# Optimization experiments

Hardware: AMD Instinct MI355X
Metric: run time of the kernel (lower is better)

## Reference

```python
import jax, jax.numpy as jnp
import numpy as np

H = 16            # num heads (sharded)
NOPE = 128        # qk_nope_head_dim
ROPE = 64         # qk_rope_head_dim
VD = 128          # v_head_dim
KV_RANK = 512
HEAD = NOPE + ROPE  # 192
SCALE = HEAD ** (-0.5)  # mscale == 1 (no yarn scaling)
EPS = 1e-6


def rmsnorm(x, w):
    var = jnp.mean(x * x, axis=-1, keepdims=True)
    return x * jax.lax.rsqrt(var + EPS) * w


def apply_rope(pe, cos, sin):
    # pe: [T, h, ROPE]; torch code de-interleaves pairs then applies
    # non-interleaved (rotate-half) rope: out = [e*cos - o*sin, o*cos + e*sin]
    e = pe[..., 0::2]
    o = pe[..., 1::2]
    c = cos[:, None, :]
    s = sin[:, None, :]
    return jnp.concatenate([e * c - o * s, o * c + e * s], axis=-1)


def setup_inputs() -> dict:
    key = jax.random.key(0)
    ks = jax.random.split(key, 10)
    T, D = 4096, 2048
    w = 0.02
    return {
        "hidden_states": jax.random.normal(ks[0], (T, D), jnp.float32),
        "cos": jax.random.uniform(ks[1], (T, ROPE // 2), jnp.float32),
        "sin": jax.random.uniform(ks[2], (T, ROPE // 2), jnp.float32),
        "w_q_a": jax.random.normal(ks[3], (D, 1536), jnp.float32) * w,
        "q_a_ln_w": jnp.ones((1536,), jnp.float32),
        "w_q_b": jax.random.normal(ks[4], (1536, H * HEAD), jnp.float32) * w,
        "w_kv_a": jax.random.normal(ks[5], (D, KV_RANK + ROPE), jnp.float32) * w,
        "kv_a_ln_w": jnp.ones((KV_RANK,), jnp.float32),
        "w_kv_b": jax.random.normal(ks[6], (KV_RANK, H * (NOPE + VD)), jnp.float32) * w,
        "w_o": jax.random.normal(ks[7], (H * VD, D), jnp.float32) * w,
        "batch_size": 2,
    }


def reference(hidden_states, cos, sin, w_q_a, q_a_ln_w, w_q_b, w_kv_a,
              kv_a_ln_w, w_kv_b, w_o, batch_size):
    T, D = hidden_states.shape
    B = int(batch_size)
    S = T // B

    # Q: low-rank down proj -> RMSNorm -> up proj
    q = rmsnorm(hidden_states @ w_q_a, q_a_ln_w) @ w_q_b
    q = q.reshape(T, H, HEAD)
    q_nope = q[..., :NOPE]
    q_pe = apply_rope(q[..., NOPE:], cos, sin)

    # KV: joint down proj with shared rope part (MQA-style)
    ckv = hidden_states @ w_kv_a                        # [T, 512+64]
    compressed_kv = ckv[:, :KV_RANK]
    k_pe = apply_rope(ckv[:, KV_RANK:][:, None, :], cos, sin)  # [T, 1, 64]
    kv = (rmsnorm(compressed_kv, kv_a_ln_w) @ w_kv_b).reshape(T, H, NOPE + VD)
    k_nope = kv[..., :NOPE]
    v = kv[..., NOPE:]                                   # [T, H, 128]

    # Assemble full query/key heads (value pad to 192 + final slice is a no-op
    # mathematically since padded dims are zero; we keep value dim = 128).
    query = jnp.concatenate([q_nope, q_pe], axis=-1)     # [T, H, 192]
    key = jnp.concatenate([k_nope, jnp.broadcast_to(k_pe, (T, H, ROPE))], axis=-1)

    # Causal (prefill) attention per sequence
    qb = query.reshape(B, S, H, HEAD)
    kb = key.reshape(B, S, H, HEAD)
    vb = v.reshape(B, S, H, VD)
    scores = jnp.einsum("bqhd,bkhd->bhqk", qb, kb) * SCALE
    causal = jnp.tril(jnp.ones((S, S), bool))
    scores = jnp.where(causal, scores, jnp.finfo(scores.dtype).min)
    probs = jax.nn.softmax(scores, axis=-1)
    attn = jnp.einsum("bhqk,bkhd->bqhd", probs, vb)      # [B, S, H, 128]

    return attn.reshape(T, H * VD) @ w_o
```

## Files before the change

kernel.cpp:

```cpp
#include <hip/hip_runtime.h>
#include <cstdint>
#include <cstddef>

#define TT 4096
#define DD 2048
#define NH 16
#define HEADD 192
#define NOPE 128
#define VDIM 128
#define SEQ 2048

typedef __bf16 bf16x8 __attribute__((ext_vector_type(8)));
typedef float f32x4 __attribute__((ext_vector_type(4)));
typedef unsigned int u32;

__device__ __forceinline__ float bf2f(unsigned short u) {
    union { unsigned int i; float f; } v; v.i = ((unsigned int)u) << 16; return v.f;
}
__device__ __forceinline__ unsigned short f2bf(float f) {
    union { float f; unsigned int i; } v; v.f = f;
    unsigned int r = v.i + 0x7FFFu + ((v.i >> 16) & 1u);
    return (unsigned short)(r >> 16);
}
__device__ __forceinline__ u32 pack2bf(float a, float b) {
    return (u32)f2bf(a) | ((u32)f2bf(b) << 16);
}
__device__ __forceinline__ void gload16(const unsigned short* g, unsigned short* l) {
    __builtin_amdgcn_global_load_lds((const __attribute__((address_space(1))) u32*)g,
                                     (__attribute__((address_space(3))) u32*)l, 16, 0, 0);
}

__global__ __launch_bounds__(256) void cvt_bf16_k(const float* __restrict__ x,
                                                  unsigned short* __restrict__ y, int n) {
    int i = (blockIdx.x * 256 + threadIdx.x) * 4;
    if (i < n) {
        float4 v = *(const float4*)(x + i);
        uint2 o;
        o.x = pack2bf(v.x, v.y);
        o.y = pack2bf(v.z, v.w);
        *(uint2*)(y + i) = o;
    }
}

__global__ __launch_bounds__(256) void transpose_cvt_k(const float* __restrict__ W,
                                                       unsigned short* __restrict__ Wt,
                                                       int K, int N) {
    __shared__ float tile[32][33];
    int n0 = blockIdx.x * 32, k0 = blockIdx.y * 32;
    int t = threadIdx.x, lr = t >> 5, lc = t & 31;
#pragma unroll
    for (int p = 0; p < 4; p++) {
        int k = k0 + lr + p * 8, n = n0 + lc;
        tile[lr + p * 8][lc] = (k < K && n < N) ? W[(size_t)k * N + n] : 0.f;
    }
    __syncthreads();
#pragma unroll
    for (int p = 0; p < 4; p++) {
        int n = n0 + lr + p * 8, k = k0 + lc;
        if (n < N && k < K) Wt[(size_t)n * K + k] = f2bf(tile[lc][lr + p * 8]);
    }
}

__global__ __launch_bounds__(256) void gemm_bf16_k(const unsigned short* __restrict__ A,
                                                   const unsigned short* __restrict__ Bt,
                                                   float* __restrict__ C,
                                                   int M, int N, int K) {
    __shared__ __align__(16) unsigned short As[128 * 32];
    __shared__ __align__(16) unsigned short Bs[128 * 32];
    int bm = blockIdx.y * 128, bn = blockIdx.x * 128;
    int t = threadIdx.x;
    int wave = t >> 6, lane = t & 63;
    int wr = (wave >> 1) * 64, wc = (wave & 1) * 64;
    int l15 = lane & 15, quad = lane >> 4;
    f32x4 acc[4][4];
    f32x4 zero = {0.f, 0.f, 0.f, 0.f};
#pragma unroll
    for (int i = 0; i < 4; i++)
#pragma unroll
        for (int j = 0; j < 4; j++) acc[i][j] = zero;
    int r0 = 16 * (2 * wave) + (lane >> 2);
    int cOff = (lane & 3) * 8;
    const unsigned short* gA0 = A + (size_t)(bm + r0) * K + cOff;
    const unsigned short* gA1 = A + (size_t)(bm + r0 + 16) * K + cOff;
    const unsigned short* gB0 = Bt + (size_t)(bn + r0) * K + cOff;
    const unsigned short* gB1 = Bt + (size_t)(bn + r0 + 16) * K + cOff;
    unsigned short* lA0 = &As[(2 * wave) * 512];
    unsigned short* lA1 = &As[(2 * wave + 1) * 512];
    unsigned short* lB0 = &Bs[(2 * wave) * 512];
    unsigned short* lB1 = &Bs[(2 * wave + 1) * 512];
    for (int k0 = 0; k0 < K; k0 += 32) {
        gload16(gA0 + k0, lA0);
        gload16(gA1 + k0, lA1);
        gload16(gB0 + k0, lB0);
        gload16(gB1 + k0, lB1);
        __syncthreads();
        bf16x8 af[4], bfr[4];
#pragma unroll
        for (int i = 0; i < 4; i++)
            af[i] = *(const bf16x8*)&As[(wr + i * 16 + l15) * 32 + quad * 8];
#pragma unroll
        for (int j = 0; j < 4; j++)
            bfr[j] = *(const bf16x8*)&Bs[(wc + j * 16 + l15) * 32 + quad * 8];
#pragma unroll
        for (int i = 0; i < 4; i++)
#pragma unroll
            for (int j = 0; j < 4; j++)
                acc[i][j] = __builtin_amdgcn_mfma_f32_16x16x32_bf16(af[i], bfr[j], acc[i][j], 0, 0, 0);
        __syncthreads();
    }
#pragma unroll
    for (int i = 0; i < 4; i++) {
        int row = bm + wr + i * 16 + quad * 4;
#pragma unroll
        for (int j = 0; j < 4; j++) {
            int col = bn + wc + j * 16 + l15;
            if (col < N) {
                float* cp = C + (size_t)row * N + col;
#pragma unroll
                for (int r = 0; r < 4; r++) cp[(size_t)r * N] = acc[i][j][r];
            }
        }
    }
}

__global__ __launch_bounds__(256) void gemm_bf16o_k(const unsigned short* __restrict__ A,
                                                    const unsigned short* __restrict__ Bt,
                                                    unsigned short* __restrict__ C,
                                                    int M, int N, int K) {
    __shared__ __align__(16) unsigned short As[128 * 32];
    __shared__ __align__(16) unsigned short Bs[128 * 32];
    int bm = blockIdx.y * 128, bn = blockIdx.x * 128;
    int t = threadIdx.x;
    int wave = t >> 6, lane = t & 63;
    int wr = (wave >> 1) * 64, wc = (wave & 1) * 64;
    int l15 = lane & 15, quad = lane >> 4;
    f32x4 acc[4][4];
    f32x4 zero = {0.f, 0.f, 0.f, 0.f};
#pragma unroll
    for (int i = 0; i < 4; i++)
#pragma unroll
        for (int j = 0; j < 4; j++) acc[i][j] = zero;
    int r0 = 16 * (2 * wave) + (lane >> 2);
    int cOff = (lane & 3) * 8;
    const unsigned short* gA0 = A + (size_t)(bm + r0) * K + cOff;
    const unsigned short* gA1 = A + (size_t)(bm + r0 + 16) * K + cOff;
    const unsigned short* gB0 = Bt + (size_t)(bn + r0) * K + cOff;
    const unsigned short* gB1 = Bt + (size_t)(bn + r0 + 16) * K + cOff;
    unsigned short* lA0 = &As[(2 * wave) * 512];
    unsigned short* lA1 = &As[(2 * wave + 1) * 512];
    unsigned short* lB0 = &Bs[(2 * wave) * 512];
    unsigned short* lB1 = &Bs[(2 * wave + 1) * 512];
    for (int k0 = 0; k0 < K; k0 += 32) {
        gload16(gA0 + k0, lA0);
        gload16(gA1 + k0, lA1);
        gload16(gB0 + k0, lB0);
        gload16(gB1 + k0, lB1);
        __syncthreads();
        bf16x8 af[4], bfr[4];
#pragma unroll
        for (int i = 0; i < 4; i++)
            af[i] = *(const bf16x8*)&As[(wr + i * 16 + l15) * 32 + quad * 8];
#pragma unroll
        for (int j = 0; j < 4; j++)
            bfr[j] = *(const bf16x8*)&Bs[(wc + j * 16 + l15) * 32 + quad * 8];
#pragma unroll
        for (int i = 0; i < 4; i++)
#pragma unroll
            for (int j = 0; j < 4; j++)
                acc[i][j] = __builtin_amdgcn_mfma_f32_16x16x32_bf16(af[i], bfr[j], acc[i][j], 0, 0, 0);
        __syncthreads();
    }
#pragma unroll
    for (int i = 0; i < 4; i++) {
        int row = bm + wr + i * 16 + quad * 4;
#pragma unroll
        for (int j = 0; j < 4; j++) {
            int col = bn + wc + j * 16 + l15;
            if (col < N) {
                unsigned short* cp = C + (size_t)row * N + col;
#pragma unroll
                for (int r = 0; r < 4; r++) cp[(size_t)r * N] = f2bf(acc[i][j][r]);
            }
        }
    }
}

#define KS_STRIDE 200
#define VT_STRIDE 72

__global__ __launch_bounds__(256) void gemm_kv_k(const unsigned short* __restrict__ A,
                                                 const unsigned short* __restrict__ Bt,
                                                 unsigned short* __restrict__ Kb2,
                                                 unsigned short* __restrict__ Vt2) {
    const int K = 512;
    __shared__ __align__(16) unsigned short As[128 * 32];
    __shared__ __align__(16) unsigned short Bs[128 * 32];
    int bm = blockIdx.y * 128, bn = blockIdx.x * 128;
    int t = threadIdx.x;
    int wave = t >> 6, lane = t & 63;
    int wr = (wave >> 1) * 64, wc = (wave & 1) * 64;
    int l15 = lane & 15, quad = lane >> 4;
    f32x4 acc[4][4];
    f32x4 zero = {0.f, 0.f, 0.f, 0.f};
#pragma unroll
    for (int i = 0; i < 4; i++)
#pragma unroll
        for (int j = 0; j < 4; j++) acc[i][j] = zero;
    int r0 = 16 * (2 * wave) + (lane >> 2);
    int cOff = (lane & 3) * 8;
    const unsigned short* gA0 = A + (size_t)(bm + r0) * K + cOff;
    const unsigned short* gA1 = A + (size_t)(bm + r0 + 16) * K + cOff;
    const unsigned short* gB0 = Bt + (size_t)(bn + r0) * K + cOff;
    const unsigned short* gB1 = Bt + (size_t)(bn + r0 + 16) * K + cOff;
    unsigned short* lA0 = &As[(2 * wave) * 512];
    unsigned short* lA1 = &As[(2 * wave + 1) * 512];
    unsigned short* lB0 = &Bs[(2 * wave) * 512];
    unsigned short* lB1 = &Bs[(2 * wave + 1) * 512];
    for (int k0 = 0; k0 < K; k0 += 32) {
        gload16(gA0 + k0, lA0);
        gload16(gA1 + k0, lA1);
        gload16(gB0 + k0, lB0);
        gload16(gB1 + k0, lB1);
        __syncthreads();
        bf16x8 af[4], bfr[4];
#pragma unroll
        for (int i = 0; i < 4; i++)
            af[i] = *(const bf16x8*)&As[(wr + i * 16 + l15) * 32 + quad * 8];
#pragma unroll
        for (int j = 0; j < 4; j++)
            bfr[j] = *(const bf16x8*)&Bs[(wc + j * 16 + l15) * 32 + quad * 8];
#pragma unroll
        for (int i = 0; i < 4; i++)
#pragma unroll
            for (int j = 0; j < 4; j++)
                acc[i][j] = __builtin_amdgcn_mfma_f32_16x16x32_bf16(af[i], bfr[j], acc[i][j], 0, 0, 0);
        __syncthreads();
    }
#pragma unroll
    for (int j = 0; j < 4; j++) {
        int col = bn + wc + j * 16 + l15;
        int h = col >> 8, dd = col & 255;
#pragma unroll
        for (int i = 0; i < 4; i++) {
            int row0 = bm + wr + i * 16 + quad * 4;
#pragma unroll
            for (int r = 0; r < 4; r++) {
                int row = row0 + r;
                int b = row >> 11, s = row & 2047;
                int kt = s >> 6, sr = s & 63;
                size_t bh = (size_t)(b * NH + h);
                unsigned short v = f2bf(acc[i][j][r]);
                if (dd < 128)
                    Kb2[((bh * 32 + kt) * 64 + sr) * KS_STRIDE + dd] = v;
                else
                    Vt2[((bh * 32 + kt) * 128 + (dd - 128)) * VT_STRIDE + sr] = v;
            }
        }
    }
}

__global__ __launch_bounds__(256) void kpe_fill_k(const unsigned short* __restrict__ kpe,
                                                  unsigned short* __restrict__ Kb2) {
    int trow = blockIdx.x, t = threadIdx.x;
    int b = trow >> 11, s = trow & 2047;
    int kt = s >> 6, sr = s & 63;
    const unsigned short* src = kpe + trow * 64;
#pragma unroll
    for (int i = t; i < NH * 64; i += 256) {
        int h = i >> 6, d = i & 63;
        Kb2[(((size_t)(b * NH + h) * 32 + kt) * 64 + sr) * KS_STRIDE + 128 + d] = src[d];
    }
}

__global__ __launch_bounds__(256) void rmsnorm_bf_k(const unsigned short* __restrict__ x,
                                                    const float* __restrict__ w,
                                                    unsigned short* __restrict__ y) {
    int row = blockIdx.x, t = threadIdx.x;
    const unsigned short* xr = x + (size_t)row * 2112;
    float s = 0.f;
    for (int i = t; i < 1536; i += 256) { float v = bf2f(xr[i]); s += v * v; }
    __shared__ float red[256];
    red[t] = s; __syncthreads();
    for (int o = 128; o > 0; o >>= 1) { if (t < o) red[t] += red[t + o]; __syncthreads(); }
    float scale = rsqrtf(red[0] / 1536.f + 1e-6f);
    unsigned short* yr = y + (size_t)row * 1536;
    for (int i = t; i < 1536; i += 256) yr[i] = f2bf(bf2f(xr[i]) * scale * w[i]);
}

__global__ __launch_bounds__(256) void kvprep_bf_k(const unsigned short* __restrict__ qab,
                                                   const float* __restrict__ w,
                                                   const float* __restrict__ cosb,
                                                   const float* __restrict__ sinb,
                                                   unsigned short* __restrict__ ckvn,
                                                   unsigned short* __restrict__ kpe) {
    int row = blockIdx.x, t = threadIdx.x;
    const unsigned short* xr = qab + (size_t)row * 2112 + 1536;
    float s = 0.f;
#pragma unroll
    for (int i = t; i < 512; i += 256) { float v = bf2f(xr[i]); s += v * v; }
    __shared__ float red[256];
    red[t] = s; __syncthreads();
    for (int o = 128; o > 0; o >>= 1) { if (t < o) red[t] += red[t + o]; __syncthreads(); }
    float scale = rsqrtf(red[0] / 512.f + 1e-6f);
    unsigned short* yr = ckvn + (size_t)row * 512;
#pragma unroll
    for (int i = t; i < 512; i += 256) yr[i] = f2bf(bf2f(xr[i]) * scale * w[i]);
    if (t < 32) {
        float e = bf2f(xr[512 + 2 * t]), o = bf2f(xr[512 + 2 * t + 1]);
        float c = cosb[row * 32 + t], sn = sinb[row * 32 + t];
        kpe[row * 64 + t]      = f2bf(e * c - o * sn);
        kpe[row * 64 + 32 + t] = f2bf(o * c + e * sn);
    }
}

__global__ __launch_bounds__(256) void qprep_bf_k(const unsigned short* __restrict__ q,
                                                  const float* __restrict__ cosb,
                                                  const float* __restrict__ sinb,
                                                  unsigned short* __restrict__ Qb) {
    const float SCALE = 0.07216878364870323f;
    int trow = blockIdx.x, t = threadIdx.x;
    const unsigned short* qr = q + (size_t)trow * (NH * HEADD);
    unsigned short* yr = Qb + (size_t)trow * (NH * HEADD);
    for (int i = t; i < NH * HEADD; i += 256) {
        int h = i / HEADD, d = i - h * HEADD;
        float val;
        if (d < NOPE) val = bf2f(qr[i]);
        else {
            int j = d - NOPE;
            int jj = j & 31;
            const unsigned short* pe = qr + h * HEADD + NOPE;
            float e = bf2f(pe[2 * jj]), o = bf2f(pe[2 * jj + 1]);
            float c = cosb[trow * 32 + jj], sn = sinb[trow * 32 + jj];
            val = (j < 32) ? (e * c - o * sn) : (o * c + e * sn);
        }
        yr[i] = f2bf(val * SCALE);
    }
}

__global__ __launch_bounds__(512) void attn_mfma_k(const unsigned short* __restrict__ Qb,
                                                   const unsigned short* __restrict__ Kb2,
                                                   const unsigned short* __restrict__ Vt2,
                                                   unsigned short* __restrict__ Opart,
                                                   float* __restrict__ Mbuf,
                                                   float* __restrict__ Lbuf) {
    __shared__ __align__(16) unsigned short Ks[64 * KS_STRIDE];
    __shared__ __align__(16) unsigned short Vts[128 * VT_STRIDE];
    int xe = 39 - blockIdx.x;
    int h  = blockIdx.y;
    int b  = blockIdx.z;
    int qt = 0, accn = 0;
    while (true) { int c = (qt >> 2) + 1; if (xe < accn + c) break; accn += c; qt++; }
    int chunk = xe - accn;
    int t = threadIdx.x;
    int w = t >> 6, lane = t & 63;
    int l15 = lane & 15, quad = lane >> 4;
    int bh = b * NH + h;
    int q0 = b * SEQ + qt * 128;
    int qglob = qt * 128 + w * 16 + l15;
    int flat = bh * 40 + xe;

    bf16x8 qf[6];
    {
        const unsigned short* qbase = Qb + ((size_t)(q0 + w * 16 + l15) * NH + h) * HEADD + quad * 8;
#pragma unroll
        for (int c = 0; c < 6; c++)
            qf[c] = *(const bf16x8*)(qbase + c * 32);
    }
    f32x4 acc_o[8];
    f32x4 zero = {0.f, 0.f, 0.f, 0.f};
#pragma unroll
    for (int j = 0; j < 8; j++) acc_o[j] = zero;
    float mrun = -1e30f, lrun = 0.f;

    int kt0 = chunk * 8, kt1 = min(kt0 + 7, 2 * qt + 1);
    int cbeg = w * 5 + min(w, 3), cnt = (w < 3) ? 6 : 5;
    for (int kt = kt0; kt <= kt1; kt++) {
        __syncthreads();
        {
            const unsigned short* kg = Kb2 + ((size_t)bh * 32 + kt) * (64 * KS_STRIDE) + lane * 8;
            const unsigned short* vg = Vt2 + ((size_t)bh * 32 + kt) * (128 * VT_STRIDE) + lane * 8;
            for (int c = cbeg; c < cbeg + cnt; c++) {
                if (c < 25) gload16(kg + c * 512, &Ks[c * 512]);
                else        gload16(vg + (c - 25) * 512, &Vts[(c - 25) * 512]);
            }
        }
        __syncthreads();
        f32x4 acc_s[4];
#pragma unroll
        for (int j = 0; j < 4; j++) acc_s[j] = zero;
#pragma unroll
        for (int c = 0; c < 6; c++) {
#pragma unroll
            for (int j = 0; j < 4; j++) {
                bf16x8 kf = *(const bf16x8*)&Ks[(j * 16 + l15) * KS_STRIDE + c * 32 + quad * 8];
                acc_s[j] = __builtin_amdgcn_mfma_f32_16x16x32_bf16(kf, qf[c], acc_s[j], 0, 0, 0);
            }
        }
        float sv[4][4];
#pragma unroll
        for (int j = 0; j < 4; j++) {
            int kbase = kt * 64 + j * 16 + quad * 4;
#pragma unroll
            for (int r = 0; r < 4; r++)
                sv[j][r] = (kbase + r > qglob) ? -1e30f : acc_s[j][r];
        }
        float v = sv[0][0];
#pragma unroll
        for (int j = 0; j < 4; j++)
#pragma unroll
            for (int r = 0; r < 4; r++) v = fmaxf(v, sv[j][r]);
        v = fmaxf(v, __shfl_xor(v, 16));
        v = fmaxf(v, __shfl_xor(v, 32));
        float mnew = fmaxf(mrun, v);
        float alpha = __expf(mrun - mnew);
        mrun = mnew;
        float rs = 0.f;
#pragma unroll
        for (int j = 0; j < 4; j++)
#pragma unroll
            for (int r = 0; r < 4; r++) { float p = __expf(sv[j][r] - mnew); sv[j][r] = p; rs += p; }
        rs += __shfl_xor(rs, 16);
        rs += __shfl_xor(rs, 32);
        lrun = lrun * alpha + rs;
        u32 pk[4][2];
#pragma unroll
        for (int j = 0; j < 4; j++) {
            pk[j][0] = pack2bf(sv[j][0], sv[j][1]);
            pk[j][1] = pack2bf(sv[j][2], sv[j][3]);
        }
#pragma unroll
        for (int jt = 0; jt < 8; jt++)
#pragma unroll
            for (int r = 0; r < 4; r++) acc_o[jt][r] *= alpha;
        int laneA = (((2 * quad) & 3) << 4) + l15;
        int laneB = (((2 * quad + 1) & 3) << 4) + l15;
        bool hi = (quad & 2) != 0;
#pragma unroll
        for (int c2 = 0; c2 < 2; c2++) {
            u32 a0 = __shfl(pk[2 * c2][0], laneA),     a1 = __shfl(pk[2 * c2][1], laneA);
            u32 b0 = __shfl(pk[2 * c2 + 1][0], laneA), b1 = __shfl(pk[2 * c2 + 1][1], laneA);
            u32 a2 = __shfl(pk[2 * c2][0], laneB),     a3 = __shfl(pk[2 * c2][1], laneB);
            u32 b2 = __shfl(pk[2 * c2 + 1][0], laneB), b3 = __shfl(pk[2 * c2 + 1][1], laneB);
            union { u32 d[4]; bf16x8 v8; } pf;
            pf.d[0] = hi ? b0 : a0;
            pf.d[1] = hi ? b1 : a1;
            pf.d[2] = hi ? b2 : a2;
            pf.d[3] = hi ? b3 : a3;
#pragma unroll
            for (int jt = 0; jt < 8; jt++) {
                bf16x8 vf = *(const bf16x8*)&Vts[(jt * 16 + l15) * VT_STRIDE + c2 * 32 + quad * 8];
                acc_o[jt] = __builtin_amdgcn_mfma_f32_16x16x32_bf16(vf, pf.v8, acc_o[jt], 0, 0, 0);
            }
        }
    }
    {
        int row = w * 16 + l15;
        unsigned short* op = Opart + (size_t)flat * 16384 + row * 128;
#pragma unroll
        for (int jt = 0; jt < 8; jt++)
#pragma unroll
            for (int r = 0; r < 4; r++)
                op[jt * 16 + quad * 4 + r] = f2bf(acc_o[jt][r]);
        if (quad == 0) {
            Mbuf[(size_t)flat * 128 + row] = mrun;
            Lbuf[(size_t)flat * 128 + row] = lrun;
        }
    }
}

__global__ __launch_bounds__(256) void attn_combine_k(const unsigned short* __restrict__ Opart,
                                                      const float* __restrict__ Mbuf,
                                                      const float* __restrict__ Lbuf,
                                                      unsigned short* __restrict__ attnb) {
    int q64 = blockIdx.x, h = blockIdx.y, b = blockIdx.z;
    int qt = q64 >> 1, half = q64 & 1;
    int nch = (qt >> 2) + 1;
    int F = 0;
    for (int q = 0; q < qt; q++) F += (q >> 2) + 1;
    int flat0 = (b * NH + h) * 40 + F;
    int t = threadIdx.x;
    int row = t >> 2, d0 = (t & 3) * 32;
    int row128 = half * 64 + row;
    float mc[4], lc[4], wgt[4];
    float mstar = -1e30f;
#pragma unroll
    for (int c = 0; c < 4; c++) {
        if (c < nch) {
            mc[c] = Mbuf[(size_t)(flat0 + c) * 128 + row128];
            lc[c] = Lbuf[(size_t)(flat0 + c) * 128 + row128];
        } else { mc[c] = -1e30f; lc[c] = 0.f; }
        mstar = fmaxf(mstar, mc[c]);
    }
    float L = 0.f;
#pragma unroll
    for (int c = 0; c < 4; c++) { wgt[c] = __expf(mc[c] - mstar); L += wgt[c] * lc[c]; }
    float invL = 1.f / L;
    float acc[32];
#pragma unroll
    for (int j = 0; j < 32; j++) acc[j] = 0.f;
#pragma unroll
    for (int c = 0; c < 4; c++) {
        if (c < nch) {
            const unsigned short* src = Opart + (size_t)(flat0 + c) * 16384 + row128 * 128 + d0;
            float wc = wgt[c];
#pragma unroll
            for (int g = 0; g < 4; g++) {
                uint4 u = *(const uint4*)(src + g * 8);
                const unsigned short* sp = (const unsigned short*)&u;
#pragma unroll
                for (int j = 0; j < 8; j++) acc[g * 8 + j] += wc * bf2f(sp[j]);
            }
        }
    }
    unsigned short* dst = attnb + (size_t)(b * SEQ + q64 * 64 + row) * 2048 + h * 128 + d0;
#pragma unroll
    for (int g = 0; g < 4; g++) {
        uint4 o;
        unsigned short* sp = (unsigned short*)&o;
#pragma unroll
        for (int j = 0; j < 8; j++) sp[j] = f2bf(acc[g * 8 + j] * invL);
        *(uint4*)(dst + g * 8) = o;
    }
}

extern "C" void kernel_launch(void* const* d_in, const int* in_sizes, int n_in,
                              void* d_out, int out_size, void* d_ws, size_t ws_size,
                              hipStream_t stream) {
    const float* hs     = (const float*)d_in[0];
    const float* cosb   = (const float*)d_in[1];
    const float* sinb   = (const float*)d_in[2];
    const float* w_q_a  = (const float*)d_in[3];
    const float* q_ln   = (const float*)d_in[4];
    const float* w_q_b  = (const float*)d_in[5];
    const float* w_kv_a = (const float*)d_in[6];
    const float* kv_ln  = (const float*)d_in[7];
    const float* w_kv_b = (const float*)d_in[8];
    const float* w_o    = (const float*)d_in[9];
    float* out = (float*)d_out;

    char* base = (char*)d_ws;
    size_t off = 0;
    auto take = [&](size_t bytes) { void* p = base + off; off += (bytes + 255) & ~(size_t)255; return p; };
    unsigned short* wqabT = (unsigned short*)take((size_t)2112 * 2048 * 2);
    unsigned short* wqbT  = (unsigned short*)take((size_t)3072 * 1536 * 2);
    unsigned short* wkvbT = (unsigned short*)take((size_t)4096 * 512 * 2);
    unsigned short* woT   = (unsigned short*)take((size_t)2048 * 2048 * 2);
    unsigned short* hsb   = (unsigned short*)take((size_t)TT * DD * 2);
    unsigned short* qab   = (unsigned short*)take((size_t)TT * 2112 * 2);
    unsigned short* qan   = (unsigned short*)take((size_t)TT * 1536 * 2);
    unsigned short* ckvn  = (unsigned short*)take((size_t)TT * 512 * 2);
    unsigned short* kpe   = (unsigned short*)take((size_t)TT * 64 * 2);
    unsigned short* qb3   = (unsigned short*)take((size_t)TT * 3072 * 2);
    unsigned short* Qbuf  = (unsigned short*)take((size_t)TT * NH * HEADD * 2);
    unsigned short* Kb2   = (unsigned short*)take((size_t)32 * 32 * 64 * KS_STRIDE * 2);
    unsigned short* Vt2   = (unsigned short*)take((size_t)32 * 32 * 128 * VT_STRIDE * 2);
    unsigned short* attnb = (unsigned short*)take((size_t)TT * 2048 * 2);
    unsigned short* Opart = (unsigned short*)take((size_t)1280 * 16384 * 2);
    float* Mbuf = (float*)take((size_t)1280 * 128 * 4);
    float* Lbuf = (float*)take((size_t)1280 * 128 * 4);

    cvt_bf16_k<<<(TT * DD) / 1024, 256, 0, stream>>>(hs, hsb, TT * DD);
    transpose_cvt_k<<<dim3(1536 / 32, 2048 / 32), 256, 0, stream>>>(w_q_a, wqabT, 2048, 1536);
    transpose_cvt_k<<<dim3(18, 2048 / 32), 256, 0, stream>>>(w_kv_a, wqabT + (size_t)1536 * 2048, 2048, 576);
    transpose_cvt_k<<<dim3(3072 / 32, 1536 / 32), 256, 0, stream>>>(w_q_b, wqbT, 1536, 3072);
    transpose_cvt_k<<<dim3(4096 / 32, 512 / 32), 256, 0, stream>>>(w_kv_b, wkvbT, 512, 4096);
    transpose_cvt_k<<<dim3(2048 / 32, 2048 / 32), 256, 0, stream>>>(w_o, woT, 2048, 2048);

    gemm_bf16o_k<<<dim3(17, 32), 256, 0, stream>>>(hsb, wqabT, qab, 4096, 2112, 2048);
    rmsnorm_bf_k<<<4096, 256, 0, stream>>>(qab, q_ln, qan);
    kvprep_bf_k<<<4096, 256, 0, stream>>>(qab, kv_ln, cosb, sinb, ckvn, kpe);
    gemm_bf16o_k<<<dim3(24, 32), 256, 0, stream>>>(qan, wqbT, qb3, 4096, 3072, 1536);
    qprep_bf_k<<<4096, 256, 0, stream>>>(qb3, cosb, sinb, Qbuf);
    gemm_kv_k<<<dim3(32, 32), 256, 0, stream>>>(ckvn, wkvbT, Kb2, Vt2);
    kpe_fill_k<<<4096, 256, 0, stream>>>(kpe, Kb2);
    attn_mfma_k<<<dim3(40, 16, 2), 512, 0, stream>>>(Qbuf, Kb2, Vt2, Opart, Mbuf, Lbuf);
    attn_combine_k<<<dim3(32, 16, 2), 256, 0, stream>>>(Opart, Mbuf, Lbuf, attnb);
    gemm_bf16_k<<<dim3(16, 32), 256, 0, stream>>>(attnb, woT, out, 4096, 2048, 2048);
}
```

Baseline: 544.2 us.

## Overlap K/V tile loads with attention compute and skip redundant rescale/mask work

```diff
diff --git a/kernel.cpp b/kernel.cpp
--- a/kernel.cpp
+++ b/kernel.cpp
@@ -28,6 +28,14 @@
 __device__ __forceinline__ void gload16(const unsigned short* g, unsigned short* l) {
     __builtin_amdgcn_global_load_lds((const __attribute__((address_space(1))) u32*)g,
                                      (__attribute__((address_space(3))) u32*)l, 16, 0, 0);
+}
+__device__ __forceinline__ void block_bar() {
+    asm volatile("" ::: "memory");
+    __builtin_amdgcn_s_barrier();
+    asm volatile("" ::: "memory");
+}
+__device__ __forceinline__ void vm_wait0() {
+    asm volatile("s_waitcnt vmcnt(0)" ::: "memory");
 }
 
 __global__ __launch_bounds__(256) void cvt_bf16_k(const float* __restrict__ x,
@@ -359,6 +367,19 @@
     int qglob = qt * 128 + w * 16 + l15;
     int flat = bh * 40 + xe;
 
+    int kt0 = chunk * 8, kt1 = min(kt0 + 7, 2 * qt + 1);
+    const bool kload = (w < 5);
+    const int kcb = w * 5;
+    const int vcb = (w - 5) * 6;
+    const unsigned short* kgbase = Kb2 + (size_t)(bh * 32) * (64 * KS_STRIDE) + lane * 8;
+    const unsigned short* vgbase = Vt2 + (size_t)(bh * 32) * (128 * VT_STRIDE) + lane * 8;
+
+    if (kload) {
+        const unsigned short* kg = kgbase + (size_t)kt0 * (64 * KS_STRIDE);
+#pragma unroll
+        for (int c = 0; c < 5; c++) gload16(kg + (kcb + c) * 512, &Ks[(kcb + c) * 512]);
+    }
+
     bf16x8 qf[6];
     {
         const unsigned short* qbase = Qb + ((size_t)(q0 + w * 16 + l15) * NH + h) * HEADD + quad * 8;
@@ -372,22 +393,19 @@
     for (int j = 0; j < 8; j++) acc_o[j] = zero;
     float mrun = -1e30f, lrun = 0.f;
 
-    int kt0 = chunk * 8, kt1 = min(kt0 + 7, 2 * qt + 1);
-    int cbeg = w * 5 + min(w, 3), cnt = (w < 3) ? 6 : 5;
+    if (kload) vm_wait0();
+    block_bar();
+    if (!kload) {
+        const unsigned short* vg = vgbase + (size_t)kt0 * (128 * VT_STRIDE);
+#pragma unroll
+        for (int c = 0; c < 6; c++) gload16(vg + (vcb + c) * 512, &Vts[(vcb + c) * 512]);
+    }
+
     for (int kt = kt0; kt <= kt1; kt++) {
-        __syncthreads();
-        {
-            const unsigned short* kg = Kb2 + ((size_t)bh * 32 + kt) * (64 * KS_STRIDE) + lane * 8;
-            const unsigned short* vg = Vt2 + ((size_t)bh * 32 + kt) * (128 * VT_STRIDE) + lane * 8;
-            for (int c = cbeg; c < cbeg + cnt; c++) {
-                if (c < 25) gload16(kg + c * 512, &Ks[c * 512]);
-                else        gload16(vg + (c - 25) * 512, &Vts[(c - 25) * 512]);
-            }
-        }
-        __syncthreads();
         f32x4 acc_s[4];
 #pragma unroll
         for (int j = 0; j < 4; j++) acc_s[j] = zero;
+        __builtin_amdgcn_s_setprio(1);
 #pragma unroll
         for (int c = 0; c < 6; c++) {
 #pragma unroll
@@ -396,13 +414,28 @@
                 acc_s[j] = __builtin_amdgcn_mfma_f32_16x16x32_bf16(kf, qf[c], acc_s[j], 0, 0, 0);
             }
         }
+        __builtin_amdgcn_s_setprio(0);
+        block_bar();
+        if (kload && kt < kt1) {
+            const unsigned short* kg = kgbase + (size_t)(kt + 1) * (64 * KS_STRIDE);
+#pragma unroll
+            for (int c = 0; c < 5; c++) gload16(kg + (kcb + c) * 512, &Ks[(kcb + c) * 512]);
+        }
         float sv[4][4];
-#pragma unroll
-        for (int j = 0; j < 4; j++) {
-            int kbase = kt * 64 + j * 16 + quad * 4;
-#pragma unroll
-            for (int r = 0; r < 4; r++)
-                sv[j][r] = (kbase + r > qglob) ? -1e30f : acc_s[j][r];
+        const bool needmask = (kt * 64 + 63) > (qt * 128 + w * 16);
+        if (needmask) {
+#pragma unroll
+            for (int j = 0; j < 4; j++) {
+                int kbase = kt * 64 + j * 16 + quad * 4;
+#pragma unroll
+                for (int r = 0; r < 4; r++)
+                    sv[j][r] = (kbase + r > qglob) ? -1e30f : acc_s[j][r];
+            }
+        } else {
+#pragma unroll
+            for (int j = 0; j < 4; j++)
+#pragma unroll
+                for (int r = 0; r < 4; r++) sv[j][r] = acc_s[j][r];
         }
         float v = sv[0][0];
 #pragma unroll
@@ -411,30 +444,34 @@
             for (int r = 0; r < 4; r++) v = fmaxf(v, sv[j][r]);
         v = fmaxf(v, __shfl_xor(v, 16));
         v = fmaxf(v, __shfl_xor(v, 32));
-        float mnew = fmaxf(mrun, v);
-        float alpha = __expf(mrun - mnew);
-        mrun = mnew;
+        if (!__all(v - mrun <= 8.f)) {
+            float mnew = fmaxf(mrun, v);
+            float alpha = __expf(mrun - mnew);
+            mrun = mnew;
+            lrun *= alpha;
+#pragma unroll
+            for (int jt = 0; jt < 8; jt++)
+#pragma unroll
+                for (int r = 0; r < 4; r++) acc_o[jt][r] *= alpha;
+        }
         float rs = 0.f;
 #pragma unroll
         for (int j = 0; j < 4; j++)
 #pragma unroll
-            for (int r = 0; r < 4; r++) { float p = __expf(sv[j][r] - mnew); sv[j][r] = p; rs += p; }
+            for (int r = 0; r < 4; r++) { float p = __expf(sv[j][r] - mrun); sv[j][r] = p; rs += p; }
         rs += __shfl_xor(rs, 16);
         rs += __shfl_xor(rs, 32);
-        lrun = lrun * alpha + rs;
+        lrun += rs;
         u32 pk[4][2];
 #pragma unroll
         for (int j = 0; j < 4; j++) {
             pk[j][0] = pack2bf(sv[j][0], sv[j][1]);
             pk[j][1] = pack2bf(sv[j][2], sv[j][3]);
         }
-#pragma unroll
-        for (int jt = 0; jt < 8; jt++)
-#pragma unroll
-            for (int r = 0; r < 4; r++) acc_o[jt][r] *= alpha;
         int laneA = (((2 * quad) & 3) << 4) + l15;
         int laneB = (((2 * quad + 1) & 3) << 4) + l15;
         bool hi = (quad & 2) != 0;
+        bf16x8 pfv[2];
 #pragma unroll
         for (int c2 = 0; c2 < 2; c2++) {
             u32 a0 = __shfl(pk[2 * c2][0], laneA),     a1 = __shfl(pk[2 * c2][1], laneA);
@@ -446,12 +483,28 @@
             pf.d[1] = hi ? b1 : a1;
             pf.d[2] = hi ? b2 : a2;
             pf.d[3] = hi ? b3 : a3;
+            pfv[c2] = pf.v8;
+        }
+        if (!kload) vm_wait0();
+        block_bar();
+        __builtin_amdgcn_s_setprio(1);
+#pragma unroll
+        for (int c2 = 0; c2 < 2; c2++) {
 #pragma unroll
             for (int jt = 0; jt < 8; jt++) {
                 bf16x8 vf = *(const bf16x8*)&Vts[(jt * 16 + l15) * VT_STRIDE + c2 * 32 + quad * 8];
-                acc_o[jt] = __builtin_amdgcn_mfma_f32_16x16x32_bf16(vf, pf.v8, acc_o[jt], 0, 0, 0);
+                acc_o[jt] = __builtin_amdgcn_mfma_f32_16x16x32_bf16(vf, pfv[c2], acc_o[jt], 0, 0, 0);
             }
         }
+        __builtin_amdgcn_s_setprio(0);
+        block_bar();
+        if (!kload && kt < kt1) {
+            const unsigned short* vg = vgbase + (size_t)(kt + 1) * (128 * VT_STRIDE);
+#pragma unroll
+            for (int c = 0; c < 6; c++) gload16(vg + (vcb + c) * 512, &Vts[(vcb + c) * 512]);
+        }
+        if (kload) vm_wait0();
+        block_bar();
     }
     {
         int row = w * 16 + l15;
```

New measurement: 561.4 us. 3.2% more time.
